# Kernel tuning notes

Measured on AMD Instinct MI355X. Metric: run time of the kernel, lower is better.

Reference implementation:

```python
import math
import jax, jax.numpy as jnp
from jax import lax
import numpy as np

STRIDES = (8, 16, 32)            # p3, p4, p5
ANCHOR_STRIDE_SCALE = 8
ASPECT_RATIOS = (0.5, 1.0, 2.0)  # A = 3
NMS_THRESH = 0.6
PRE_NMS_TOPK = 400
POST_NMS_TOPK = 50
BBOX_CLAMP = 4.135166556742356   # log(1000/16)


def setup_inputs() -> dict:
    key = jax.random.key(0)
    ks = jax.random.split(key, 8)
    C = 256
    inp = {
        "p3": jax.random.normal(ks[0], (8, C, 128, 128), jnp.float32),
        "p4": jax.random.normal(ks[1], (8, C, 64, 64), jnp.float32),
        "p5": jax.random.normal(ks[2], (8, C, 32, 32), jnp.float32),
        # fan-in scaled weights so logits/deltas stay in a sane range
        "w_stem": jax.random.normal(ks[3], (C, C, 3, 3), jnp.float32) * (1.0 / math.sqrt(C * 9)),
        "b_stem": jnp.zeros((C,), jnp.float32),
        "w_obj": jax.random.normal(ks[4], (3, C, 1, 1), jnp.float32) * (1.0 / math.sqrt(C)),
        "b_obj": jnp.zeros((3,), jnp.float32),
        "w_box": jax.random.normal(ks[5], (12, C, 1, 1), jnp.float32) * (0.01 / math.sqrt(C)),
        "b_box": jnp.zeros((12,), jnp.float32),
    }
    return inp


def _conv(x, w, b, pad):
    y = lax.conv_general_dilated(x, w, (1, 1), pad,
                                 dimension_numbers=("NCHW", "OIHW", "NCHW"))
    return y + b[None, :, None, None]


def _make_anchors(H, W, stride):
    # anchor centers at (x+0.5)*stride ; base size = stride * anchor_stride_scale
    xs = (jnp.arange(W, dtype=jnp.float32) + 0.5) * stride
    ys = (jnp.arange(H, dtype=jnp.float32) + 0.5) * stride
    cx, cy = jnp.meshgrid(xs, ys)              # (H, W), row-major matches H*W flatten
    cx = cx.reshape(-1)
    cy = cy.reshape(-1)
    size = float(stride * ANCHOR_STRIDE_SCALE)
    per_ratio = []
    for r in ASPECT_RATIOS:
        w = size / math.sqrt(r)
        h = size * math.sqrt(r)
        per_ratio.append(jnp.stack([cx - w / 2, cy - h / 2, cx + w / 2, cy + h / 2], axis=-1))
    return jnp.stack(per_ratio, axis=1).reshape(-1, 4)  # (H*W*A, 4)


def _decode(deltas, anchors):
    aw = anchors[:, 2] - anchors[:, 0]
    ah = anchors[:, 3] - anchors[:, 1]
    acx = anchors[:, 0] + 0.5 * aw
    acy = anchors[:, 1] + 0.5 * ah
    dx, dy = deltas[:, 0], deltas[:, 1]
    dw = jnp.clip(deltas[:, 2], -BBOX_CLAMP, BBOX_CLAMP)
    dh = jnp.clip(deltas[:, 3], -BBOX_CLAMP, BBOX_CLAMP)
    pcx = acx + dx * aw
    pcy = acy + dy * ah
    pw = aw * jnp.exp(dw)
    ph = ah * jnp.exp(dh)
    return jnp.stack([pcx - 0.5 * pw, pcy - 0.5 * ph,
                      pcx + 0.5 * pw, pcy + 0.5 * ph], axis=-1)


def _nms_keep(boxes, thresh):
    # boxes already sorted by descending score; greedy class-agnostic NMS
    N = boxes.shape[0]
    x1, y1, x2, y2 = boxes[:, 0], boxes[:, 1], boxes[:, 2], boxes[:, 3]
    area = jnp.maximum(x2 - x1, 0.0) * jnp.maximum(y2 - y1, 0.0)
    ix1 = jnp.maximum(x1[:, None], x1[None, :])
    iy1 = jnp.maximum(y1[:, None], y1[None, :])
    ix2 = jnp.minimum(x2[:, None], x2[None, :])
    iy2 = jnp.minimum(y2[:, None], y2[None, :])
    inter = jnp.maximum(ix2 - ix1, 0.0) * jnp.maximum(iy2 - iy1, 0.0)
    iou = inter / jnp.maximum(area[:, None] + area[None, :] - inter, 1e-8)  # (N, N)
    idx = jnp.arange(N)

    def body(keep, i):
        suppress = (iou[i] > thresh) & keep[i] & (idx > i)
        return keep & ~suppress, 0

    keep, _ = lax.scan(body, jnp.ones((N,), bool), idx)
    return keep


def _proposals_one_image(logits, deltas, anchors):
    # logits: (N,), deltas: (N, 4), anchors: (N, 4)
    k = min(PRE_NMS_TOPK, logits.shape[0])
    scores, top_idx = lax.top_k(logits, k)
    boxes = _decode(deltas[top_idx], anchors[top_idx])
    keep = _nms_keep(boxes, NMS_THRESH)
    masked = jnp.where(keep, scores, -jnp.inf)
    _, kidx = lax.top_k(masked, POST_NMS_TOPK)
    return boxes[kidx]  # (POST_NMS_TOPK, 4)


def _rpn_level(feat, w_stem, b_stem, w_obj, b_obj, w_box, b_box, stride):
    B, _, H, W = feat.shape
    x = jax.nn.relu(_conv(feat, w_stem, b_stem, "SAME"))       # stem: 3x3 conv + ReLU
    obj = _conv(x, w_obj, b_obj, "VALID")                      # (B, A, H, W)
    box = _conv(x, w_box, b_box, "VALID")                      # (B, 4A, H, W)
    A = obj.shape[1]
    obj = obj.transpose(0, 2, 3, 1).reshape(B, H * W * A)       # (B, HWA)
    box = box.transpose(0, 2, 3, 1).reshape(B, H * W * A, 4)    # (B, HWA, 4)
    anchors = _make_anchors(H, W, stride)                       # (HWA, 4)
    return jax.vmap(lambda o, d: _proposals_one_image(o, d, anchors))(obj, box)


def reference(p3, p4, p5, w_stem, b_stem, w_obj, b_obj, w_box, b_box):
    out = []
    for feat, stride in zip((p3, p4, p5), STRIDES):
        out.append(_rpn_level(feat, w_stem, b_stem, w_obj, b_obj, w_box, b_box, stride))
    # (B, 3 * POST_NMS_TOPK, 4) absolute XYXY proposals, concatenated across levels
    return jnp.concatenate(out, axis=1)
```

## Files before the change

### kernel.cpp

```cpp
#include <hip/hip_runtime.h>
#include <math.h>
#include <stdint.h>

#define BBOX_CLAMP 4.135166556742356f
#define SQH 0.70710678118654752f
#define SQ2 1.41421356237309515f

typedef __attribute__((ext_vector_type(8))) short s8b;
typedef __attribute__((ext_vector_type(4))) float f32x4;
typedef __attribute__((ext_vector_type(4))) short s4b;

__device__ __forceinline__ unsigned okey(float f){
  unsigned u = __float_as_uint(f);
  return (u & 0x80000000u) ? ~u : (u | 0x80000000u);
}
__device__ __forceinline__ unsigned short f2bf(float f){
  unsigned u = __float_as_uint(f);
  unsigned r = (u + 0x7FFFu + ((u >> 16) & 1u)) >> 16;
  return (unsigned short)r;
}
__device__ __forceinline__ float bf2f(unsigned short h){
  return __uint_as_float(((unsigned)h) << 16);
}

__global__ void k_wsplit(const float* __restrict__ w,
                         unsigned short* __restrict__ whi, unsigned short* __restrict__ wlo){
  const int ck = blockIdx.x;
  const int cout = threadIdx.x;
  const int cin = ck / 9, tap = ck - cin*9;
  const float x = w[cout*2304 + ck];
  const unsigned short h = f2bf(x);
  const unsigned short lo2 = f2bf(x - bf2f(h));
  const int slice = cin >> 5, g = (cin >> 3) & 3, j = cin & 7;
  const size_t off = ((((size_t)tap*8 + slice)*4 + g)*256 + cout)*8 + j;
  whi[off] = h; wlo[off] = lo2;
}

__global__ __launch_bounds__(256, 2) void k_stem_mfma(
    const float* __restrict__ p3f, const float* __restrict__ p4f, const float* __restrict__ p5f,
    const unsigned short* __restrict__ whi, const unsigned short* __restrict__ wlo,
    const float* __restrict__ bstem,
    const float* __restrict__ wobj, const float* __restrict__ bobj,
    const float* __restrict__ wbox, const float* __restrict__ bbox,
    float* __restrict__ sc3, float* __restrict__ dl3,
    float* __restrict__ sc4, float* __restrict__ dl4,
    float* __restrict__ sc5, float* __restrict__ dl5)
{
  __shared__ __align__(16) unsigned char smem[34816];
  unsigned short* Abuf = reinterpret_cast<unsigned short*>(smem);
  float* part = reinterpret_cast<float*>(smem);

  const int tid = threadIdx.x;
  const int l = tid & 63, w = tid >> 6;
  const int li = l & 15, g = l >> 4;

  int id = blockIdx.x;
  const float* feat; float* scores; float* deltas; int H, W, bx, by, b;
  if (id < 1024){ feat=p3f; scores=sc3; deltas=dl3; H=128; W=128;
      bx = id & 3; by = (id >> 2) & 31; b = id >> 7; }
  else if (id < 1280){ id -= 1024; feat=p4f; scores=sc4; deltas=dl4; H=64; W=64;
      bx = id & 1; by = (id >> 1) & 15; b = id >> 5; }
  else { id -= 1280; feat=p5f; scores=sc5; deltas=dl5; H=32; W=32;
      bx = 0; by = id & 7; b = id >> 3; }
  const int px0 = bx*32, py0 = by*4;
  const size_t HW = (size_t)H*W;
  const float* fb = feat + (size_t)b*256*HW;

  const int gr = tid / 34, gc = tid - gr*34;
  const int row = py0 + gr - 1, col = px0 + gc - 1;
  const bool inb = (tid < 204) && row >= 0 && row < H && col >= 0 && col < W;
  const bool lact = (tid < 204);
  const float* gA = fb + ((size_t)(inb ? row : 0)*W + (inb ? col : 0));

  f32x4 acc[8][4];
#pragma unroll
  for (int m=0;m<8;++m)
#pragma unroll
    for (int cg=0;cg<4;++cg) acc[m][cg] = (f32x4){0.f,0.f,0.f,0.f};

  const int lig = li*40 + g*8;

  for (int slice = 0; slice < 8; ++slice){
    __syncthreads();
    const float* gs = gA + (size_t)slice*32*HW;
#pragma unroll
    for (int ch = 0; ch < 8; ++ch){
      float x0=0.f, x1=0.f, x2=0.f, x3=0.f;
      if (inb){
        x0 = gs[(size_t)(ch*4+0)*HW];
        x1 = gs[(size_t)(ch*4+1)*HW];
        x2 = gs[(size_t)(ch*4+2)*HW];
        x3 = gs[(size_t)(ch*4+3)*HW];
      }
      if (lact){
        const unsigned short h0=f2bf(x0), h1=f2bf(x1), h2=f2bf(x2), h3=f2bf(x3);
        s4b hv; hv[0]=(short)h0; hv[1]=(short)h1; hv[2]=(short)h2; hv[3]=(short)h3;
        s4b lv; lv[0]=(short)f2bf(x0-bf2f(h0)); lv[1]=(short)f2bf(x1-bf2f(h1));
                lv[2]=(short)f2bf(x2-bf2f(h2)); lv[3]=(short)f2bf(x3-bf2f(h3));
        *reinterpret_cast<s4b*>(&Abuf[tid*40 + ch*4]) = hv;
        *reinterpret_cast<s4b*>(&Abuf[8160 + tid*40 + ch*4]) = lv;
      }
    }
    __syncthreads();

    for (int tap = 0; tap < 9; ++tap){
      const int dr = tap/3 - 1, dc = tap - (tap/3)*3 - 1;
      s8b bh[4], bl[4];
#pragma unroll
      for (int cg = 0; cg < 4; ++cg){
        const int woff = ((((tap*8 + slice)*4 + g)*256) + (w*64 + cg*16 + li))*8;
        bh[cg] = *reinterpret_cast<const s8b*>(&whi[woff]);
        bl[cg] = *reinterpret_cast<const s8b*>(&wlo[woff]);
      }
      const int tb = (dr*34 + dc)*40;
#pragma unroll
      for (int m = 0; m < 8; ++m){
        const int rm = m >> 1, cm = m & 1;
        const int aoff = ((rm+1)*34 + cm*16 + 1)*40 + lig + tb;
        const s8b ahi = *reinterpret_cast<const s8b*>(&Abuf[aoff]);
        const s8b alo = *reinterpret_cast<const s8b*>(&Abuf[8160 + aoff]);
#pragma unroll
        for (int cg = 0; cg < 4; ++cg)
          acc[m][cg] = __builtin_amdgcn_mfma_f32_16x16x32_bf16(ahi, bh[cg], acc[m][cg], 0, 0, 0);
#pragma unroll
        for (int cg = 0; cg < 4; ++cg)
          acc[m][cg] = __builtin_amdgcn_mfma_f32_16x16x32_bf16(ahi, bl[cg], acc[m][cg], 0, 0, 0);
#pragma unroll
        for (int cg = 0; cg < 4; ++cg)
          acc[m][cg] = __builtin_amdgcn_mfma_f32_16x16x32_bf16(alo, bh[cg], acc[m][cg], 0, 0, 0);
      }
    }
  }

#pragma unroll
  for (int cg = 0; cg < 4; ++cg){
    const float bsv = bstem[w*64 + cg*16 + li];
#pragma unroll
    for (int m = 0; m < 8; ++m)
#pragma unroll
      for (int r = 0; r < 4; ++r)
        acc[m][cg][r] = fmaxf(acc[m][cg][r] + bsv, 0.f);
  }

  __syncthreads();

#pragma unroll
  for (int oc = 0; oc < 15; ++oc){
    float wv[4];
#pragma unroll
    for (int cg = 0; cg < 4; ++cg){
      const int cc = w*64 + cg*16 + li;
      wv[cg] = (oc < 3) ? wobj[oc*256 + cc] : wbox[(oc-3)*256 + cc];
    }
#pragma unroll
    for (int m = 0; m < 8; ++m){
#pragma unroll
      for (int r = 0; r < 4; ++r){
        float t = acc[m][0][r] * wv[0];
        t = fmaf(acc[m][1][r], wv[1], t);
        t = fmaf(acc[m][2][r], wv[2], t);
        t = fmaf(acc[m][3][r], wv[3], t);
        t += __shfl_xor(t, 1, 64);
        t += __shfl_xor(t, 2, 64);
        t += __shfl_xor(t, 4, 64);
        t += __shfl_xor(t, 8, 64);
        if (li == 0){
          const int rm = m >> 1, cm = m & 1;
          const int px = rm*32 + cm*16 + g*4 + r;
          part[(w*128 + px)*17 + oc] = t;
        }
      }
    }
  }
  __syncthreads();

  {
    const int px = tid & 127, half = tid >> 7;
    const int rm2 = px >> 5, rem = px & 31;
    const int hh = py0 + rm2, ww = px0 + rem;
    const size_t loc = (size_t)hh*W + ww;
    const int oce = half ? 15 : 8;
    for (int oc = half*8; oc < oce; ++oc){
      float s = ((part[(0*128+px)*17+oc] + part[(1*128+px)*17+oc])
               +  part[(2*128+px)*17+oc]) + part[(3*128+px)*17+oc];
      s += (oc < 3) ? bobj[oc] : bbox[oc-3];
      if (oc < 3) scores[(size_t)b*HW*3 + loc*3 + oc] = s;
      else        deltas[(size_t)b*HW*12 + loc*12 + (oc-3)] = s;
    }
  }
}

__global__ __launch_bounds__(1024) void k_select(
    const float* __restrict__ sc3, const float* __restrict__ sc4, const float* __restrict__ sc5,
    const float* __restrict__ dl3, const float* __restrict__ dl4, const float* __restrict__ dl5,
    float* __restrict__ out)
{
  const int lvl = blockIdx.x >> 3;
  const int b   = blockIdx.x & 7;
  int N, W; float stride; const float* sc; const float* dl;
  if (lvl==0){ N=49152; W=128; stride=8.f;  sc=sc3; dl=dl3; }
  else if (lvl==1){ N=12288; W=64; stride=16.f; sc=sc4; dl=dl4; }
  else { N=3072; W=32; stride=32.f; sc=sc5; dl=dl5; }
  sc += (size_t)b*N;
  dl += (size_t)b*(size_t)(N/3)*12;

  __shared__ unsigned hist[256];
  __shared__ unsigned s_prefix;
  __shared__ int s_need;
  __shared__ int s_cntc;
  __shared__ unsigned long long cand[1024];
  __shared__ int tk[400];
  __shared__ float bx1[400], by1[400], bx2[400], by2[400], bar_[400];
  __shared__ unsigned long long mask[400][7];
  __shared__ int olist[50];

  const int t = threadIdx.x;

  if (t==0){ s_prefix=0u; s_need=400; }
  for (int pass=0; pass<4; ++pass){
    const int shift = 24 - 8*pass;
    if (t<256) hist[t]=0u;
    __syncthreads();
    const unsigned pref = s_prefix;
    for (int i=t; i<N; i+=1024){
      const unsigned k = okey(sc[i]);
      if (pass==0 || (k >> (shift+8)) == pref)
        atomicAdd(&hist[(k>>shift)&255u], 1u);
    }
    __syncthreads();
    if (t==0){
      int need = s_need, cum=0, bsel=0;
      for (int bb=255; bb>=0; --bb){
        const int h = (int)hist[bb];
        if (cum + h >= need){ bsel=bb; break; }
        cum += h;
      }
      s_prefix = (pref<<8) | (unsigned)bsel;
      s_need = need - cum;
    }
    __syncthreads();
  }
  const unsigned K = s_prefix;

  if (t==0) s_cntc = 0;
  cand[t] = 0ull;
  __syncthreads();
  for (int i=t; i<N; i+=1024){
    const unsigned k = okey(sc[i]);
    if (k >= K){
      const int pos = atomicAdd(&s_cntc, 1);
      if (pos < 1024)
        cand[pos] = ((unsigned long long)k<<32) | (unsigned long long)(0xFFFFFFFFu - (unsigned)i);
    }
  }
  __syncthreads();

  for (int kk=2; kk<=1024; kk<<=1){
    for (int j=kk>>1; j>0; j>>=1){
      const int ixj = t ^ j;
      if (ixj > t){
        const unsigned long long a = cand[t], c = cand[ixj];
        const bool descending = ((t & kk) == 0);
        if ((a < c) == descending){ cand[t]=c; cand[ixj]=a; }
      }
      __syncthreads();
    }
  }

  if (t < 400){
    const unsigned long long c = cand[t];
    const int gi = (int)(0xFFFFFFFFu - (unsigned)(c & 0xFFFFFFFFull));
    tk[t] = gi;
    const int loc = gi/3, a = gi - loc*3;
    const int hh = loc / W, ww = loc - hh*W;
    const float cx = (ww + 0.5f)*stride, cy = (hh + 0.5f)*stride;
    const float size = stride*8.f;
    const float sq = (a==0) ? SQH : ((a==1) ? 1.f : SQ2);
    const float hw_ = 0.5f*(size/sq);
    const float hv_ = 0.5f*(size*sq);
    const float ax1 = cx - hw_, ax2 = cx + hw_;
    const float ay1 = cy - hv_, ay2 = cy + hv_;
    const float aw = ax2 - ax1, ah = ay2 - ay1;
    const float acx = ax1 + 0.5f*aw, acy = ay1 + 0.5f*ah;
    const float* dd = dl + (size_t)loc*12 + a*4;
    const float dx = dd[0], dy = dd[1];
    const float dw = fminf(fmaxf(dd[2], -BBOX_CLAMP), BBOX_CLAMP);
    const float dh = fminf(fmaxf(dd[3], -BBOX_CLAMP), BBOX_CLAMP);
    const float pcx = acx + dx*aw;
    const float pcy = acy + dy*ah;
    const float pw = aw*expf(dw);
    const float ph = ah*expf(dh);
    const float x1 = pcx - 0.5f*pw, y1 = pcy - 0.5f*ph;
    const float x2 = pcx + 0.5f*pw, y2 = pcy + 0.5f*ph;
    bx1[t]=x1; by1[t]=y1; bx2[t]=x2; by2[t]=y2;
    bar_[t] = fmaxf(x2-x1, 0.f)*fmaxf(y2-y1, 0.f);
  }
  __syncthreads();

  for (int task=t; task<2800; task+=1024){
    const int i = task/7, w = task - (task/7)*7;
    unsigned long long m = 0ull;
    const float xi1=bx1[i], yi1=by1[i], xi2=bx2[i], yi2=by2[i], ai=bar_[i];
    const int j0 = w<<6;
    const int js = (j0 > i+1) ? j0 : (i+1);
    const int je = (j0+64 < 400) ? (j0+64) : 400;
    for (int j=js; j<je; ++j){
      const float ix1 = fmaxf(xi1, bx1[j]);
      const float iy1 = fmaxf(yi1, by1[j]);
      const float ix2 = fminf(xi2, bx2[j]);
      const float iy2 = fminf(yi2, by2[j]);
      const float inter = fmaxf(ix2-ix1, 0.f)*fmaxf(iy2-iy1, 0.f);
      const float iou = inter / fmaxf(ai + bar_[j] - inter, 1e-8f);
      if (iou > 0.6f) m |= (1ull << (j - j0));
    }
    mask[i][w] = m;
  }
  __syncthreads();

  if (t==0){
    unsigned long long keepw[7];
#pragma unroll
    for (int w=0;w<7;++w) keepw[w] = ~0ull;
    for (int i=0;i<400;++i){
      if ((keepw[i>>6] >> (i&63)) & 1ull){
#pragma unroll
        for (int w=0;w<7;++w) keepw[w] &= ~mask[i][w];
      }
    }
    int cnt=0;
    for (int i=0;i<400 && cnt<50;++i) if ( (keepw[i>>6]>>(i&63)) & 1ull) olist[cnt++]=i;
    for (int i=0;i<400 && cnt<50;++i) if (!((keepw[i>>6]>>(i&63)) & 1ull)) olist[cnt++]=i;
  }
  __syncthreads();

  if (t < 50){
    const int j = olist[t];
    float* o = out + (size_t)b*600 + (size_t)(lvl*50 + t)*4;
    o[0]=bx1[j]; o[1]=by1[j]; o[2]=bx2[j]; o[3]=by2[j];
  }
}

extern "C" void kernel_launch(void* const* d_in, const int* in_sizes, int n_in,
                              void* d_out, int out_size, void* d_ws, size_t ws_size,
                              hipStream_t stream) {
  (void)in_sizes; (void)n_in; (void)out_size; (void)ws_size;
  const float* p3     = (const float*)d_in[0];
  const float* p4     = (const float*)d_in[1];
  const float* p5     = (const float*)d_in[2];
  const float* w_stem = (const float*)d_in[3];
  const float* b_stem = (const float*)d_in[4];
  const float* w_obj  = (const float*)d_in[5];
  const float* b_obj  = (const float*)d_in[6];
  const float* w_box  = (const float*)d_in[7];
  const float* b_box  = (const float*)d_in[8];
  float* out = (float*)d_out;

  unsigned short* whi = (unsigned short*)d_ws;
  unsigned short* wlo = whi + 589824;
  float* sc3 = (float*)(wlo + 589824);
  float* sc4 = sc3 + 393216;
  float* sc5 = sc4 + 98304;
  float* dl3 = sc5 + 24576;
  float* dl4 = dl3 + 1572864;
  float* dl5 = dl4 + 393216;

  k_wsplit<<<dim3(2304), dim3(256), 0, stream>>>(w_stem, whi, wlo);

  k_stem_mfma<<<dim3(1344), dim3(256), 0, stream>>>(
      p3, p4, p5, whi, wlo, b_stem, w_obj, b_obj, w_box, b_box,
      sc3, dl3, sc4, dl4, sc5, dl5);

  k_select<<<dim3(24), dim3(1024), 0, stream>>>(sc3, sc4, sc5, dl3, dl4, dl5, out);
}
```

Before: 833.3 us.

## Double-buffer stem conv input slices in LDS and prefetch next slice during MFMA

The 3x3 stem conv kernel now keeps two LDS buffers for the bf16 hi/lo split of each 32-channel input slice. While MFMAs run on the current slice, the first 8 channels of the next slice are loaded into registers. The rest are loaded and converted after the tap loop, which removes one barrier per slice. LDS use grows from 34 KB to about 64 KB per block, which may cut occupancy below the launch_bounds target of 2 blocks per CU and adds register pressure from the prefetched values.

```diff
diff --git a/kernel.cpp b/kernel.cpp
--- a/kernel.cpp
+++ b/kernel.cpp
@@ -46,7 +46,7 @@
     float* __restrict__ sc4, float* __restrict__ dl4,
     float* __restrict__ sc5, float* __restrict__ dl5)
 {
-  __shared__ __align__(16) unsigned char smem[34816];
+  __shared__ __align__(16) unsigned char smem[65280];
   unsigned short* Abuf = reinterpret_cast<unsigned short*>(smem);
   float* part = reinterpret_cast<float*>(smem);
 
@@ -80,29 +80,39 @@
 
   const int lig = li*40 + g*8;
 
+#pragma unroll
+  for (int ch = 0; ch < 8; ++ch){
+    float x0=0.f, x1=0.f, x2=0.f, x3=0.f;
+    if (inb){
+      x0 = gA[(size_t)(ch*4+0)*HW];
+      x1 = gA[(size_t)(ch*4+1)*HW];
+      x2 = gA[(size_t)(ch*4+2)*HW];
+      x3 = gA[(size_t)(ch*4+3)*HW];
+    }
+    if (lact){
+      const unsigned short h0=f2bf(x0), h1=f2bf(x1), h2=f2bf(x2), h3=f2bf(x3);
+      s4b hv; hv[0]=(short)h0; hv[1]=(short)h1; hv[2]=(short)h2; hv[3]=(short)h3;
+      s4b lv; lv[0]=(short)f2bf(x0-bf2f(h0)); lv[1]=(short)f2bf(x1-bf2f(h1));
+              lv[2]=(short)f2bf(x2-bf2f(h2)); lv[3]=(short)f2bf(x3-bf2f(h3));
+      *reinterpret_cast<s4b*>(&Abuf[tid*40 + ch*4]) = hv;
+      *reinterpret_cast<s4b*>(&Abuf[8160 + tid*40 + ch*4]) = lv;
+    }
+  }
+  __syncthreads();
+
   for (int slice = 0; slice < 8; ++slice){
-    __syncthreads();
-    const float* gs = gA + (size_t)slice*32*HW;
-#pragma unroll
-    for (int ch = 0; ch < 8; ++ch){
-      float x0=0.f, x1=0.f, x2=0.f, x3=0.f;
-      if (inb){
-        x0 = gs[(size_t)(ch*4+0)*HW];
-        x1 = gs[(size_t)(ch*4+1)*HW];
-        x2 = gs[(size_t)(ch*4+2)*HW];
-        x3 = gs[(size_t)(ch*4+3)*HW];
-      }
-      if (lact){
-        const unsigned short h0=f2bf(x0), h1=f2bf(x1), h2=f2bf(x2), h3=f2bf(x3);
-        s4b hv; hv[0]=(short)h0; hv[1]=(short)h1; hv[2]=(short)h2; hv[3]=(short)h3;
-        s4b lv; lv[0]=(short)f2bf(x0-bf2f(h0)); lv[1]=(short)f2bf(x1-bf2f(h1));
-                lv[2]=(short)f2bf(x2-bf2f(h2)); lv[3]=(short)f2bf(x3-bf2f(h3));
-        *reinterpret_cast<s4b*>(&Abuf[tid*40 + ch*4]) = hv;
-        *reinterpret_cast<s4b*>(&Abuf[8160 + tid*40 + ch*4]) = lv;
-      }
-    }
-    __syncthreads();
-
+    const int buf = slice & 1;
+    const unsigned short* Ab = Abuf + buf*16320;
+    unsigned short* An = Abuf + (buf^1)*16320;
+    const float* gn = gA + (size_t)(slice+1)*32*HW;
+
+    float pv0=0.f,pv1=0.f,pv2=0.f,pv3=0.f,pv4=0.f,pv5=0.f,pv6=0.f,pv7=0.f;
+    if (slice < 7 && inb){
+      pv0 = gn[0*HW]; pv1 = gn[1*HW]; pv2 = gn[2*HW]; pv3 = gn[3*HW];
+      pv4 = gn[4*HW]; pv5 = gn[5*HW]; pv6 = gn[6*HW]; pv7 = gn[7*HW];
+    }
+
+#pragma unroll 3
     for (int tap = 0; tap < 9; ++tap){
       const int dr = tap/3 - 1, dc = tap - (tap/3)*3 - 1;
       s8b bh[4], bl[4];
@@ -117,8 +127,8 @@
       for (int m = 0; m < 8; ++m){
         const int rm = m >> 1, cm = m & 1;
         const int aoff = ((rm+1)*34 + cm*16 + 1)*40 + lig + tb;
-        const s8b ahi = *reinterpret_cast<const s8b*>(&Abuf[aoff]);
-        const s8b alo = *reinterpret_cast<const s8b*>(&Abuf[8160 + aoff]);
+        const s8b ahi = *reinterpret_cast<const s8b*>(&Ab[aoff]);
+        const s8b alo = *reinterpret_cast<const s8b*>(&Ab[8160 + aoff]);
 #pragma unroll
         for (int cg = 0; cg < 4; ++cg)
           acc[m][cg] = __builtin_amdgcn_mfma_f32_16x16x32_bf16(ahi, bh[cg], acc[m][cg], 0, 0, 0);
@@ -130,6 +140,42 @@
           acc[m][cg] = __builtin_amdgcn_mfma_f32_16x16x32_bf16(alo, bh[cg], acc[m][cg], 0, 0, 0);
       }
     }
+
+    if (slice < 7){
+      if (lact){
+        const unsigned short h0=f2bf(pv0), h1=f2bf(pv1), h2=f2bf(pv2), h3=f2bf(pv3);
+        s4b hv; hv[0]=(short)h0; hv[1]=(short)h1; hv[2]=(short)h2; hv[3]=(short)h3;
+        s4b lv; lv[0]=(short)f2bf(pv0-bf2f(h0)); lv[1]=(short)f2bf(pv1-bf2f(h1));
+                lv[2]=(short)f2bf(pv2-bf2f(h2)); lv[3]=(short)f2bf(pv3-bf2f(h3));
+        *reinterpret_cast<s4b*>(&An[tid*40 + 0]) = hv;
+        *reinterpret_cast<s4b*>(&An[8160 + tid*40 + 0]) = lv;
+        const unsigned short h4=f2bf(pv4), h5=f2bf(pv5), h6=f2bf(pv6), h7=f2bf(pv7);
+        s4b hv2; hv2[0]=(short)h4; hv2[1]=(short)h5; hv2[2]=(short)h6; hv2[3]=(short)h7;
+        s4b lv2; lv2[0]=(short)f2bf(pv4-bf2f(h4)); lv2[1]=(short)f2bf(pv5-bf2f(h5));
+                 lv2[2]=(short)f2bf(pv6-bf2f(h6)); lv2[3]=(short)f2bf(pv7-bf2f(h7));
+        *reinterpret_cast<s4b*>(&An[tid*40 + 4]) = hv2;
+        *reinterpret_cast<s4b*>(&An[8160 + tid*40 + 4]) = lv2;
+      }
+#pragma unroll
+      for (int ch = 2; ch < 8; ++ch){
+        float x0=0.f, x1=0.f, x2=0.f, x3=0.f;
+        if (inb){
+          x0 = gn[(size_t)(ch*4+0)*HW];
+          x1 = gn[(size_t)(ch*4+1)*HW];
+          x2 = gn[(size_t)(ch*4+2)*HW];
+          x3 = gn[(size_t)(ch*4+3)*HW];
+        }
+        if (lact){
+          const unsigned short h0=f2bf(x0), h1=f2bf(x1), h2=f2bf(x2), h3=f2bf(x3);
+          s4b hv; hv[0]=(short)h0; hv[1]=(short)h1; hv[2]=(short)h2; hv[3]=(short)h3;
+          s4b lv; lv[0]=(short)f2bf(x0-bf2f(h0)); lv[1]=(short)f2bf(x1-bf2f(h1));
+                  lv[2]=(short)f2bf(x2-bf2f(h2)); lv[3]=(short)f2bf(x3-bf2f(h3));
+          *reinterpret_cast<s4b*>(&An[tid*40 + ch*4]) = hv;
+          *reinterpret_cast<s4b*>(&An[8160 + tid*40 + ch*4]) = lv;
+        }
+      }
+    }
+    __syncthreads();
   }
 
 #pragma unroll
```

Measured after the change: 855.8 us. 1.03x slower.
